# Kernel tuning notes

Hardware: AMD Instinct MI355X
Metric: run time of the kernel (lower is better)

The kernel has to match this reference:

```python
import jax, jax.numpy as jnp
import numpy as np

B, T, N, F_, KH, D, KD = 16, 12, 325, 64, 4, 16, 3  # batch, time, nodes, feat, heads, head_dim, diffusion steps
H = KH // 2
EPS = 1e-5


def setup_inputs() -> dict:
    key = jax.random.key(0)
    ks = jax.random.split(key, 16)
    lin = lambda k: (jax.random.normal(k, (F_, F_), jnp.float32) * 0.02)
    return {
        "x": jax.random.normal(ks[0], (B, T, N, F_), jnp.float32),
        "A": jax.random.uniform(ks[1], (KD, N, N), jnp.float32),
        "AT": jax.random.uniform(ks[2], (KD, N, N), jnp.float32),
        "Wq": lin(ks[3]), "bq": jnp.zeros((F_,), jnp.float32),
        "Wk": lin(ks[4]), "bk": jnp.zeros((F_,), jnp.float32),
        "Wks": lin(ks[5]), "bks": jnp.zeros((F_,), jnp.float32),
        "Wv": lin(ks[6]), "bv": jnp.zeros((F_,), jnp.float32),
        "Wvs": lin(ks[7]), "bvs": jnp.zeros((F_,), jnp.float32),
        "Wdi": jax.random.normal(ks[8], (H, KD, N, N), jnp.float32) * 0.05,
        "Wdo": jax.random.normal(ks[9], (H, KD, N, N), jnp.float32) * 0.05,
        "Wf1": lin(ks[10]), "bf1": jnp.zeros((F_,), jnp.float32),
        "Wf2": lin(ks[11]), "bf2": jnp.zeros((F_,), jnp.float32),
        "g_ln": jnp.ones((F_,), jnp.float32), "b_ln": jnp.zeros((F_,), jnp.float32),
    }


def _heads(y):
    # [B,T,N,F] -> [KH,B,T,N,D]  (torch.split along -1 then stack on dim 0)
    return y.reshape(B, T, N, KH, D).transpose(3, 0, 1, 2, 4)


def _attn_half(q, k, ks_, v, vs, bias):
    # q,k,ks_,v,vs: [H,B,T,N,D]; bias: [H,1,1,N,N]
    scale = 1.0 / jnp.sqrt(jnp.float32(D))
    e = jnp.einsum('hbtnd,hbtmd->hbtnm', q, k) * scale + bias
    es = jax.nn.sigmoid((q * ks_).sum(-1, keepdims=True) * scale)  # [H,B,T,N,1]
    e = e - e.max(-1, keepdims=True)
    ex = jnp.exp(e)
    a = ex / (es + ex.sum(-1, keepdims=True))  # sigmoid-augmented softmax
    out = jnp.einsum('hbtnm,hbtmd->hbtnd', a, v)
    return out + vs - a.sum(-1, keepdims=True) * vs


def reference(x, A, AT, Wq, bq, Wk, bk, Wks, bks, Wv, bv, Wvs, bvs,
              Wdi, Wdo, Wf1, bf1, Wf2, bf2, g_ln, b_ln):
    q = _heads(x @ Wq.T + bq)
    k = _heads(x @ Wk.T + bk)
    ks_ = _heads(x @ Wks.T + bks)
    v = _heads(x @ Wv.T + bv)
    vs = _heads(x @ Wvs.T + bvs)

    # DCN graph-diffusion bias: sum_j W[h,j] * A[j] -> [H,1,1,N,N]
    bias_i = jnp.einsum('hknm,knm->hnm', Wdi, A)[:, None, None]
    bias_o = jnp.einsum('hknm,knm->hnm', Wdo, AT)[:, None, None]

    vi = _attn_half(q[:H], k[:H], ks_[:H], v[:H], vs[:H], bias_i)
    vo = _attn_half(q[H:], k[H:], ks_[H:], v[H:], vs[H:], bias_o)

    val = jnp.concatenate([vi, vo], 0)  # [KH,B,T,N,D]
    val = val.transpose(1, 2, 3, 0, 4).reshape(B, T, N, F_)

    h = jax.nn.gelu(val @ Wf1.T + bf1, approximate=False) @ Wf2.T + bf2
    h = h + x

    mu = h.mean(-1, keepdims=True)
    var = ((h - mu) ** 2).mean(-1, keepdims=True)
    return g_ln * (h - mu) / jnp.sqrt(var + EPS) + b_ln
```

## Files before the change

kernel.cpp:

```cpp
#include <hip/hip_runtime.h>
#include <hip/hip_bf16.h>
#include <math.h>

#define NN 325
#define FD 64
#define KH 4
#define DH 16
#define BT 192
#define NN2 (NN*NN)
#define PST (NN*DH)
#define SSTR 340
#define BSTR 352
#define VTS  352
#define VSLICE (16*VTS)
#define HSTR 72
#define NPROJ 975
#define NBIAS ((KH*NN*BSTR + 255)/256)
#define NPAD  (KH*BT)
#define LOG2E 1.44269504088896f

typedef __attribute__((ext_vector_type(8))) short short8;
typedef __attribute__((ext_vector_type(4))) float f32x4;

union U8 { uint4 u; short8 s; ushort us[8]; };
__device__ inline short8 lds8(const ushort* p){ U8 t; t.u = *(const uint4*)p; return t.s; }
__device__ inline float b2f(ushort v){ return __uint_as_float(((unsigned)v) << 16); }
__device__ inline ushort f2b(float f){
  unsigned u = __float_as_uint(f);
  u += 0x7fff + ((u >> 16) & 1);
  return (ushort)(u >> 16);
}
__device__ inline unsigned pk2(float a, float b){
  union { __hip_bfloat162 h; unsigned u; } t;
  t.h = __float22bfloat162_rn(float2{a, b});
  return t.u;
}
__device__ inline short8 cvt8(const float* p){
  float4 u = ((const float4*)p)[0], v = ((const float4*)p)[1];
  U8 t;
  t.us[0]=f2b(u.x); t.us[1]=f2b(u.y); t.us[2]=f2b(u.z); t.us[3]=f2b(u.w);
  t.us[4]=f2b(v.x); t.us[5]=f2b(v.y); t.us[6]=f2b(v.z); t.us[7]=f2b(v.w);
  return t.s;
}

__global__ __launch_bounds__(256) void wpack_kernel(
    const float* __restrict__ Wq,  const float* __restrict__ bq,
    const float* __restrict__ Wk,  const float* __restrict__ bk,
    const float* __restrict__ Wks, const float* __restrict__ bks,
    const float* __restrict__ Wv,  const float* __restrict__ bv,
    const float* __restrict__ Wvs, const float* __restrict__ bvs,
    const float* __restrict__ Wf1, const float* __restrict__ Wf2,
    ushort* __restrict__ Wcat, float* __restrict__ bcat){
  int blk = blockIdx.x;
  const float* Ws[7] = {Wq, Wk, Wks, Wv, Wvs, Wf1, Wf2};
  const float* bs[5] = {bq, bk, bks, bv, bvs};
  int f = blk * 64 + (threadIdx.x >> 2);
  int c0 = (threadIdx.x & 3) * 8;
  const float* wr = Ws[blk] + (f & 63) * 64;
  unsigned* dst = (unsigned*)Wcat + f * 32 + c0;
  #pragma unroll
  for (int c = 0; c < 8; ++c)
    dst[c] = f2b(wr[2*(c0+c)]) | ((unsigned)f2b(wr[2*(c0+c)+1]) << 16);
  if (blk < 5 && (threadIdx.x & 3) == 0) bcat[f] = bs[blk][f & 63];
}

__global__ __launch_bounds__(256) void prep_kernel(
    const float* __restrict__ x, const ushort* __restrict__ Wcat,
    const float* __restrict__ bcat, ushort* __restrict__ proj,
    ushort* __restrict__ vt,
    const float* __restrict__ Wdi, const float* __restrict__ Wdo,
    const float* __restrict__ A,   const float* __restrict__ AT,
    float* __restrict__ biasP){
  int bid = blockIdx.x, tid = threadIdx.x;
  if (bid < NPROJ){
    int lane = tid & 63, wid = tid >> 6;
    int r0 = bid * 64 + wid * 16;
    int m = lane & 15, g = lane >> 4;
    int gr = r0 + m;
    int bt = gr / NN, n = gr - bt * NN;
    const float* xr = x + (size_t)gr * 64 + g * 8;
    short8 xb0 = cvt8(xr);
    short8 xb1 = cvt8(xr + 32);
    for (int ct = 0; ct < 20; ++ct){
      short8 w0 = lds8(Wcat + ((size_t)(ct*16 + m) * 64 + g * 8));
      short8 w1 = lds8(Wcat + ((size_t)(ct*16 + m) * 64 + g * 8 + 32));
      float4 b4 = *(const float4*)(bcat + ct*16 + 4*g);
      f32x4 acc = {b4.x, b4.y, b4.z, b4.w};
      acc = __builtin_amdgcn_mfma_f32_16x16x32_bf16(w0, xb0, acc, 0, 0, 0);
      acc = __builtin_amdgcn_mfma_f32_16x16x32_bf16(w1, xb1, acc, 0, 0, 0);
      if (ct >= 12 && ct < 16){
        ushort* vs = vt + (size_t)((ct-12)*BT + bt) * VSLICE + n;
        #pragma unroll
        for (int rg = 0; rg < 4; ++rg)
          vs[(size_t)(4*g + rg) * VTS] = f2b(acc[rg]);
      } else {
        float sc = (ct < 4) ? 0.25f * LOG2E : 1.0f;
        uint2 w;
        w.x = pk2(acc[0]*sc, acc[1]*sc);
        w.y = pk2(acc[2]*sc, acc[3]*sc);
        *(uint2*)(proj + ((size_t)ct * BT + bt) * PST + n*16 + 4*g) = w;
      }
    }
  } else if (bid < NPROJ + NBIAS){
    int idx = (bid - NPROJ) * 256 + tid;
    if (idx >= KH * NN * BSTR) return;
    int h = idx / (NN * BSTR), rem = idx - h * (NN * BSTR);
    int n = rem / BSTR, m = rem - n * BSTR;
    float s = -1e30f;
    if (m < NN){
      int r = n * NN + m;
      s = 0.f;
      if (h < 2){
        #pragma unroll
        for (int k = 0; k < 3; ++k) s += Wdi[(h*3 + k)*NN2 + r] * A[k*NN2 + r];
      } else {
        int h2 = h - 2;
        #pragma unroll
        for (int k = 0; k < 3; ++k) s += Wdo[(h2*3 + k)*NN2 + r] * AT[k*NN2 + r];
      }
      s *= LOG2E;
    }
    biasP[idx] = s;
  } else {
    int slice = bid - NPROJ - NBIAS;
    ushort* vs = vt + (size_t)slice * VSLICE;
    if (tid < 432){
      int d = tid / 27, c = NN + tid % 27;
      vs[(size_t)d * VTS + c] = 0;
    }
  }
}

__global__ __launch_bounds__(256, 4) void attn_kernel(
    const ushort* __restrict__ proj, const float* __restrict__ biasP,
    const ushort* __restrict__ vt, ushort* __restrict__ val){
  __shared__ float S[16 * SSTR];
  __shared__ float part[4][16][16];
  __shared__ float rstat[16][2];
  int bhid = blockIdx.x, qt = blockIdx.y;
  int h = bhid / BT, bt = bhid - h * BT;
  int tid = threadIdx.x, lane = tid & 63, wid = tid >> 6;
  const ushort* qb  = proj + (size_t)((0*KH + h)*BT + bt) * PST;
  const ushort* kb  = proj + (size_t)((1*KH + h)*BT + bt) * PST;
  const ushort* ksb = proj + (size_t)((2*KH + h)*BT + bt) * PST;
  const ushort* vsb = proj + (size_t)((4*KH + h)*BT + bt) * PST;
  const ushort* vtg = vt + (size_t)(h*BT + bt) * VSLICE;

  int m = lane & 15, g = lane >> 4;
  short8 zero = {0,0,0,0,0,0,0,0};

  short8 aq = (g < 2) ? lds8(qb + ((size_t)(qt*16 + m) * 16 + g * 8)) : zero;
  short8 kf[6];
  #pragma unroll
  for (int i = 0; i < 6; ++i){
    int ct = wid + 4*i;
    kf[i] = (ct < 21 && g < 2) ? lds8(kb + ((size_t)(ct*16 + m) * 16 + g * 8)) : zero;
  }
  short8 vf[3];
  #pragma unroll
  for (int i = 0; i < 3; ++i){
    int tt = wid + 4*i;
    vf[i] = (tt < 11) ? lds8(vtg + (size_t)m * VTS + tt*32 + g*8) : zero;
  }
  int r = tid >> 4, c = tid & 15;
  int n = qt * 16 + r;
  int nb = min(n, NN - 1);
  const float* bp = biasP + (size_t)(h*NN + nb) * BSTR;
  float4 b4[6];
  #pragma unroll
  for (int j = 0; j < 6; ++j){
    int m0 = c * 4 + 64 * j;
    b4[j] = (m0 < 336) ? *(const float4*)(bp + m0) : make_float4(0.f,0.f,0.f,0.f);
  }
  float qv  = b2f(qb[(size_t)nb * 16 + c]);
  float kv  = b2f(ksb[(size_t)nb * 16 + c]);
  float vsv = b2f(vsb[(size_t)nb * 16 + c]);

  #pragma unroll
  for (int i = 0; i < 6; ++i){
    int ct = wid + 4*i;
    if (ct < 21){
      f32x4 acc = {0.f, 0.f, 0.f, 0.f};
      acc = __builtin_amdgcn_mfma_f32_16x16x32_bf16(aq, kf[i], acc, 0, 0, 0);
      #pragma unroll
      for (int rg = 0; rg < 4; ++rg)
        S[(g*4 + rg)*SSTR + ct*16 + m] = acc[rg];
    }
  }
  __syncthreads();

  {
    float* sr = S + r * SSTR;
    ushort* pr = (ushort*)sr;
    float sum = 0.f;
    #pragma unroll
    for (int j = 0; j < 6; ++j){
      int m0 = c * 4 + 64 * j;
      if (m0 < 336){
        float4 s4 = *(const float4*)(sr + m0);
        float e0 = __builtin_amdgcn_exp2f(s4.x + b4[j].x);
        float e1 = __builtin_amdgcn_exp2f(s4.y + b4[j].y);
        float e2 = __builtin_amdgcn_exp2f(s4.z + b4[j].z);
        float e3 = __builtin_amdgcn_exp2f(s4.w + b4[j].w);
        sum += (e0 + e1) + (e2 + e3);
        uint2 w;
        w.x = pk2(e0, e1);
        w.y = pk2(e2, e3);
        *(uint2*)(pr + m0) = w;
      }
    }
    float dp = qv * kv;
    dp += __shfl_xor(dp, 1, 64); dp += __shfl_xor(dp, 2, 64);
    dp += __shfl_xor(dp, 4, 64); dp += __shfl_xor(dp, 8, 64);
    sum += __shfl_xor(sum, 1, 64); sum += __shfl_xor(sum, 2, 64);
    sum += __shfl_xor(sum, 4, 64); sum += __shfl_xor(sum, 8, 64);
    if (c == 0){
      float esv = __builtin_amdgcn_rcpf(1.f + __builtin_amdgcn_exp2f(-dp));
      float iv  = __builtin_amdgcn_rcpf(esv + sum);
      rstat[r][0] = iv; rstat[r][1] = 1.f - sum * iv;
    }
  }
  __syncthreads();

  {
    const ushort* prow = (const ushort*)S + (size_t)m * (SSTR * 2);
    f32x4 acc = {0.f, 0.f, 0.f, 0.f};
    #pragma unroll
    for (int i = 0; i < 3; ++i){
      int tt = wid + 4*i;
      if (tt < 11){
        short8 ap = (tt == 10 && g >= 2) ? zero : lds8(prow + tt*32 + g*8);
        acc = __builtin_amdgcn_mfma_f32_16x16x32_bf16(ap, vf[i], acc, 0, 0, 0);
      }
    }
    #pragma unroll
    for (int rg = 0; rg < 4; ++rg)
      part[wid][g*4 + rg][m] = acc[rg];
  }
  __syncthreads();

  if (n < NN){
    float s = part[0][r][c] + part[1][r][c] + part[2][r][c] + part[3][r][c];
    float res = s * rstat[r][0] + rstat[r][1] * vsv;
    val[((size_t)bt * NN + n) * FD + h * 16 + c] = f2b(res);
  }
}

__global__ __launch_bounds__(256) void ffn_kernel(
    const ushort* __restrict__ val, const float* __restrict__ x,
    const ushort* __restrict__ Wf1b, const float* __restrict__ bf1,
    const ushort* __restrict__ Wf2b, const float* __restrict__ bf2,
    const float* __restrict__ g_ln, const float* __restrict__ b_ln,
    float* __restrict__ out){
  __shared__ ushort hs[4][16 * HSTR];
  int tid = threadIdx.x, lane = tid & 63, wid = tid >> 6;
  int m = lane & 15, g = lane >> 4;
  int r0 = blockIdx.x * 64 + wid * 16;
  int row = r0 + m;

  short8 vb0 = lds8(val + ((size_t)row * 64 + g * 8));
  short8 vb1 = lds8(val + ((size_t)row * 64 + g * 8 + 32));

  #pragma unroll
  for (int ct = 0; ct < 4; ++ct){
    short8 w0 = lds8(Wf1b + ((size_t)(ct*16 + m) * 64 + g * 8));
    short8 w1 = lds8(Wf1b + ((size_t)(ct*16 + m) * 64 + g * 8 + 32));
    float4 b4 = *(const float4*)(bf1 + ct*16 + 4*g);
    f32x4 acc = {b4.x, b4.y, b4.z, b4.w};
    acc = __builtin_amdgcn_mfma_f32_16x16x32_bf16(w0, vb0, acc, 0, 0, 0);
    acc = __builtin_amdgcn_mfma_f32_16x16x32_bf16(w1, vb1, acc, 0, 0, 0);
    uint2 w;
    float g0 = 0.5f*acc[0]*(1.f + erff(acc[0]*0.70710678118654752f));
    float g1 = 0.5f*acc[1]*(1.f + erff(acc[1]*0.70710678118654752f));
    float g2 = 0.5f*acc[2]*(1.f + erff(acc[2]*0.70710678118654752f));
    float g3 = 0.5f*acc[3]*(1.f + erff(acc[3]*0.70710678118654752f));
    w.x = pk2(g0, g1); w.y = pk2(g2, g3);
    *(uint2*)&hs[wid][m * HSTR + ct*16 + 4*g] = w;
  }
  asm volatile("s_waitcnt lgkmcnt(0)" ::: "memory");
  short8 h0 = lds8(&hs[wid][m * HSTR + g * 8]);
  short8 h1 = lds8(&hs[wid][m * HSTR + g * 8 + 32]);

  float t[4][4];
  #pragma unroll
  for (int ct = 0; ct < 4; ++ct){
    short8 w0 = lds8(Wf2b + ((size_t)(ct*16 + m) * 64 + g * 8));
    short8 w1 = lds8(Wf2b + ((size_t)(ct*16 + m) * 64 + g * 8 + 32));
    float4 b4 = *(const float4*)(bf2 + ct*16 + 4*g);
    f32x4 acc = {b4.x, b4.y, b4.z, b4.w};
    acc = __builtin_amdgcn_mfma_f32_16x16x32_bf16(w0, h0, acc, 0, 0, 0);
    acc = __builtin_amdgcn_mfma_f32_16x16x32_bf16(w1, h1, acc, 0, 0, 0);
    float4 xr = *(const float4*)(x + (size_t)row * 64 + ct*16 + 4*g);
    t[ct][0] = acc[0] + xr.x; t[ct][1] = acc[1] + xr.y;
    t[ct][2] = acc[2] + xr.z; t[ct][3] = acc[3] + xr.w;
  }
  float s = 0.f;
  #pragma unroll
  for (int ct = 0; ct < 4; ++ct) s += (t[ct][0]+t[ct][1]) + (t[ct][2]+t[ct][3]);
  s += __shfl_xor(s, 16, 64); s += __shfl_xor(s, 32, 64);
  float mu = s * (1.f/64.f);
  float v = 0.f;
  #pragma unroll
  for (int ct = 0; ct < 4; ++ct){
    #pragma unroll
    for (int rg = 0; rg < 4; ++rg){ float d = t[ct][rg] - mu; v += d*d; }
  }
  v += __shfl_xor(v, 16, 64); v += __shfl_xor(v, 32, 64);
  float rs = rsqrtf(v * (1.f/64.f) + 1e-5f);
  #pragma unroll
  for (int ct = 0; ct < 4; ++ct){
    float4 g4 = *(const float4*)(g_ln + ct*16 + 4*g);
    float4 bb = *(const float4*)(b_ln + ct*16 + 4*g);
    float4 o;
    o.x = g4.x*(t[ct][0]-mu)*rs + bb.x;
    o.y = g4.y*(t[ct][1]-mu)*rs + bb.y;
    o.z = g4.z*(t[ct][2]-mu)*rs + bb.z;
    o.w = g4.w*(t[ct][3]-mu)*rs + bb.w;
    *(float4*)(out + (size_t)row * 64 + ct*16 + 4*g) = o;
  }
}

extern "C" void kernel_launch(void* const* d_in, const int* in_sizes, int n_in,
                              void* d_out, int out_size, void* d_ws, size_t ws_size,
                              hipStream_t stream) {
  const float* x    = (const float*)d_in[0];
  const float* A    = (const float*)d_in[1];
  const float* AT   = (const float*)d_in[2];
  const float* Wq   = (const float*)d_in[3];
  const float* bq   = (const float*)d_in[4];
  const float* Wk   = (const float*)d_in[5];
  const float* bk   = (const float*)d_in[6];
  const float* Wks  = (const float*)d_in[7];
  const float* bks  = (const float*)d_in[8];
  const float* Wv   = (const float*)d_in[9];
  const float* bv   = (const float*)d_in[10];
  const float* Wvs  = (const float*)d_in[11];
  const float* bvs  = (const float*)d_in[12];
  const float* Wdi  = (const float*)d_in[13];
  const float* Wdo  = (const float*)d_in[14];
  const float* Wf1  = (const float*)d_in[15];
  const float* bf1  = (const float*)d_in[16];
  const float* Wf2  = (const float*)d_in[17];
  const float* bf2  = (const float*)d_in[18];
  const float* g_ln = (const float*)d_in[19];
  const float* b_ln = (const float*)d_in[20];
  float* out = (float*)d_out;

  float* ws = (float*)d_ws;
  ushort* proj  = (ushort*)ws;
  float*  biasP = ws + 9984000;
  ushort* val   = (ushort*)(ws + 10441600);
  ushort* vt    = (ushort*)(ws + 12438400);
  ushort* Wcat  = (ushort*)(ws + 14601088);
  float*  bcat  = ws + 14615424;
  ushort* Wf1b  = Wcat + 320*64;
  ushort* Wf2b  = Wcat + 384*64;

  wpack_kernel<<<7, 256, 0, stream>>>(Wq, bq, Wk, bk, Wks, bks,
                                      Wv, bv, Wvs, bvs, Wf1, Wf2, Wcat, bcat);
  prep_kernel<<<NPROJ + NBIAS + NPAD, 256, 0, stream>>>(
      x, Wcat, bcat, proj, vt, Wdi, Wdo, A, AT, biasP);
  attn_kernel<<<dim3(KH*BT, 21), 256, 0, stream>>>(proj, biasP, vt, val);
  ffn_kernel<<<975, 256, 0, stream>>>(val, x, Wf1b, bf1, Wf2b, bf2,
                                      g_ln, b_ln, out);
}
```

Baseline: 197.0 us.

## Fold bias into QK MFMA via identity operand, one wave per query tile

The attention kernel now gives each wave its own 16-row query tile and computes scores with a single MFMA per column tile. The K dimension's upper half multiplies a precomputed bf16 identity matrix by the bf16 graph bias, so the bias add is folded into the matrix multiply. Scores are exponentiated directly from registers into per-wave LDS, and the block-wide barriers and cross-wave partial reductions are removed. The bias is now stored as bf16 instead of fp32, which halves its traffic but lowers the precision of the bias term.

```diff
diff --git a/kernel.cpp b/kernel.cpp
--- a/kernel.cpp
+++ b/kernel.cpp
@@ -9,13 +9,12 @@
 #define BT 192
 #define NN2 (NN*NN)
 #define PST (NN*DH)
-#define SSTR 340
-#define BSTR 352
 #define VTS  352
 #define VSLICE (16*VTS)
 #define HSTR 72
+#define PLW 352
 #define NPROJ 975
-#define NBIAS ((KH*NN*BSTR + 255)/256)
+#define NBIAS 1848
 #define NPAD  (KH*BT)
 #define LOG2E 1.44269504088896f
 
@@ -50,8 +49,19 @@
     const float* __restrict__ Wv,  const float* __restrict__ bv,
     const float* __restrict__ Wvs, const float* __restrict__ bvs,
     const float* __restrict__ Wf1, const float* __restrict__ Wf2,
-    ushort* __restrict__ Wcat, float* __restrict__ bcat){
+    ushort* __restrict__ Wcat, float* __restrict__ bcat,
+    ushort* __restrict__ idT){
   int blk = blockIdx.x;
+  if (blk == 7){
+    for (int e = threadIdx.x; e < 672; e += 256){
+      int l = e & 31, mm = l & 15, gg = l >> 4;
+      U8 t;
+      #pragma unroll
+      for (int j = 0; j < 8; ++j) t.us[j] = (mm == gg*8 + j) ? (ushort)0x3F80 : (ushort)0;
+      *(uint4*)(idT + (size_t)e*8) = t.u;
+    }
+    return;
+  }
   const float* Ws[7] = {Wq, Wk, Wks, Wv, Wvs, Wf1, Wf2};
   const float* bs[5] = {bq, bk, bks, bv, bvs};
   int f = blk * 64 + (threadIdx.x >> 2);
@@ -70,7 +80,7 @@
     ushort* __restrict__ vt,
     const float* __restrict__ Wdi, const float* __restrict__ Wdo,
     const float* __restrict__ A,   const float* __restrict__ AT,
-    float* __restrict__ biasP){
+    ushort* __restrict__ biasB){
   int bid = blockIdx.x, tid = threadIdx.x;
   if (bid < NPROJ){
     int lane = tid & 63, wid = tid >> 6;
@@ -103,12 +113,12 @@
     }
   } else if (bid < NPROJ + NBIAS){
     int idx = (bid - NPROJ) * 256 + tid;
-    if (idx >= KH * NN * BSTR) return;
-    int h = idx / (NN * BSTR), rem = idx - h * (NN * BSTR);
-    int n = rem / BSTR, m = rem - n * BSTR;
+    int h = idx / 118272;
+    int rem = idx - h * 118272;
+    int n = rem / 352, mc = rem - n * 352;
     float s = -1e30f;
-    if (m < NN){
-      int r = n * NN + m;
+    if (n < NN && mc < NN){
+      int r = n * NN + mc;
       s = 0.f;
       if (h < 2){
         #pragma unroll
@@ -120,7 +130,7 @@
       }
       s *= LOG2E;
     }
-    biasP[idx] = s;
+    biasB[idx] = f2b(s);
   } else {
     int slice = bid - NPROJ - NBIAS;
     ushort* vs = vt + (size_t)slice * VSLICE;
@@ -131,118 +141,88 @@
   }
 }
 
-__global__ __launch_bounds__(256, 4) void attn_kernel(
-    const ushort* __restrict__ proj, const float* __restrict__ biasP,
-    const ushort* __restrict__ vt, ushort* __restrict__ val){
-  __shared__ float S[16 * SSTR];
-  __shared__ float part[4][16][16];
-  __shared__ float rstat[16][2];
-  int bhid = blockIdx.x, qt = blockIdx.y;
-  int h = bhid / BT, bt = bhid - h * BT;
+__global__ __launch_bounds__(256, 3) void attn_kernel(
+    const ushort* __restrict__ proj, const ushort* __restrict__ biasB,
+    const ushort* __restrict__ idT, const ushort* __restrict__ vt,
+    ushort* __restrict__ val){
+  __shared__ __align__(16) ushort Pl[4][16*PLW];
   int tid = threadIdx.x, lane = tid & 63, wid = tid >> 6;
+  int tile = blockIdx.x * 4 + wid;
+  int qt = tile % 21, bh = tile / 21;
+  int h = bh / BT, bt = bh - h * BT;
+  int m = lane & 15, g = lane >> 4;
+
   const ushort* qb  = proj + (size_t)((0*KH + h)*BT + bt) * PST;
   const ushort* kb  = proj + (size_t)((1*KH + h)*BT + bt) * PST;
   const ushort* ksb = proj + (size_t)((2*KH + h)*BT + bt) * PST;
   const ushort* vsb = proj + (size_t)((4*KH + h)*BT + bt) * PST;
-  const ushort* vtg = vt + (size_t)(h*BT + bt) * VSLICE;
-
-  int m = lane & 15, g = lane >> 4;
-  short8 zero = {0,0,0,0,0,0,0,0};
-
-  short8 aq = (g < 2) ? lds8(qb + ((size_t)(qt*16 + m) * 16 + g * 8)) : zero;
-  short8 kf[6];
-  #pragma unroll
-  for (int i = 0; i < 6; ++i){
-    int ct = wid + 4*i;
-    kf[i] = (ct < 21 && g < 2) ? lds8(kb + ((size_t)(ct*16 + m) * 16 + g * 8)) : zero;
-  }
-  short8 vf[3];
-  #pragma unroll
-  for (int i = 0; i < 3; ++i){
-    int tt = wid + 4*i;
-    vf[i] = (tt < 11) ? lds8(vtg + (size_t)m * VTS + tt*32 + g*8) : zero;
-  }
-  int r = tid >> 4, c = tid & 15;
-  int n = qt * 16 + r;
-  int nb = min(n, NN - 1);
-  const float* bp = biasP + (size_t)(h*NN + nb) * BSTR;
-  float4 b4[6];
-  #pragma unroll
-  for (int j = 0; j < 6; ++j){
-    int m0 = c * 4 + 64 * j;
-    b4[j] = (m0 < 336) ? *(const float4*)(bp + m0) : make_float4(0.f,0.f,0.f,0.f);
-  }
-  float qv  = b2f(qb[(size_t)nb * 16 + c]);
-  float kv  = b2f(ksb[(size_t)nb * 16 + c]);
-  float vsv = b2f(vsb[(size_t)nb * 16 + c]);
-
-  #pragma unroll
-  for (int i = 0; i < 6; ++i){
-    int ct = wid + 4*i;
-    if (ct < 21){
-      f32x4 acc = {0.f, 0.f, 0.f, 0.f};
-      acc = __builtin_amdgcn_mfma_f32_16x16x32_bf16(aq, kf[i], acc, 0, 0, 0);
-      #pragma unroll
-      for (int rg = 0; rg < 4; ++rg)
-        S[(g*4 + rg)*SSTR + ct*16 + m] = acc[rg];
-    }
-  }
-  __syncthreads();
-
-  {
-    float* sr = S + r * SSTR;
-    ushort* pr = (ushort*)sr;
-    float sum = 0.f;
-    #pragma unroll
-    for (int j = 0; j < 6; ++j){
-      int m0 = c * 4 + 64 * j;
-      if (m0 < 336){
-        float4 s4 = *(const float4*)(sr + m0);
-        float e0 = __builtin_amdgcn_exp2f(s4.x + b4[j].x);
-        float e1 = __builtin_amdgcn_exp2f(s4.y + b4[j].y);
-        float e2 = __builtin_amdgcn_exp2f(s4.z + b4[j].z);
-        float e3 = __builtin_amdgcn_exp2f(s4.w + b4[j].w);
-        sum += (e0 + e1) + (e2 + e3);
-        uint2 w;
-        w.x = pk2(e0, e1);
-        w.y = pk2(e2, e3);
-        *(uint2*)(pr + m0) = w;
-      }
-    }
-    float dp = qv * kv;
-    dp += __shfl_xor(dp, 1, 64); dp += __shfl_xor(dp, 2, 64);
-    dp += __shfl_xor(dp, 4, 64); dp += __shfl_xor(dp, 8, 64);
-    sum += __shfl_xor(sum, 1, 64); sum += __shfl_xor(sum, 2, 64);
-    sum += __shfl_xor(sum, 4, 64); sum += __shfl_xor(sum, 8, 64);
-    if (c == 0){
-      float esv = __builtin_amdgcn_rcpf(1.f + __builtin_amdgcn_exp2f(-dp));
-      float iv  = __builtin_amdgcn_rcpf(esv + sum);
-      rstat[r][0] = iv; rstat[r][1] = 1.f - sum * iv;
-    }
-  }
-  __syncthreads();
-
-  {
-    const ushort* prow = (const ushort*)S + (size_t)m * (SSTR * 2);
+
+  const ushort* pa0 = (g < 2) ? (kb + m*16 + g*8) : (idT + (size_t)(lane & 31)*8);
+  const ushort* pb0 = (g < 2)
+      ? (qb + (size_t)(qt*16 + m)*16 + g*8)
+      : (biasB + (size_t)(h*336 + qt*16 + m)*352 + (g-2)*8);
+  int bstep = (g < 2) ? 0 : 16;
+
+  ushort* Pw = &Pl[wid][m*PLW + g*4];
+  float rowsum = 0.f;
+  #pragma unroll
+  for (int ct = 0; ct < 21; ++ct){
+    short8 a = lds8(pa0 + ct*256);
+    short8 b = lds8(pb0 + ct*bstep);
     f32x4 acc = {0.f, 0.f, 0.f, 0.f};
-    #pragma unroll
-    for (int i = 0; i < 3; ++i){
-      int tt = wid + 4*i;
-      if (tt < 11){
-        short8 ap = (tt == 10 && g >= 2) ? zero : lds8(prow + tt*32 + g*8);
-        acc = __builtin_amdgcn_mfma_f32_16x16x32_bf16(ap, vf[i], acc, 0, 0, 0);
-      }
-    }
-    #pragma unroll
-    for (int rg = 0; rg < 4; ++rg)
-      part[wid][g*4 + rg][m] = acc[rg];
-  }
-  __syncthreads();
-
-  if (n < NN){
-    float s = part[0][r][c] + part[1][r][c] + part[2][r][c] + part[3][r][c];
-    float res = s * rstat[r][0] + rstat[r][1] * vsv;
-    val[((size_t)bt * NN + n) * FD + h * 16 + c] = f2b(res);
+    acc = __builtin_amdgcn_mfma_f32_16x16x32_bf16(a, b, acc, 0, 0, 0);
+    float e0 = __builtin_amdgcn_exp2f(acc[0]);
+    float e1 = __builtin_amdgcn_exp2f(acc[1]);
+    float e2 = __builtin_amdgcn_exp2f(acc[2]);
+    float e3 = __builtin_amdgcn_exp2f(acc[3]);
+    rowsum += (e0 + e1) + (e2 + e3);
+    uint2 w; w.x = pk2(e0, e1); w.y = pk2(e2, e3);
+    *(uint2*)(Pw + ct*16) = w;
+  }
+  { uint2 z; z.x = 0u; z.y = 0u; *(uint2*)(Pw + 336) = z; }
+
+  rowsum += __shfl_xor(rowsum, 16, 64);
+  rowsum += __shfl_xor(rowsum, 32, 64);
+
+  int nq = qt*16 + m, nb = min(nq, NN-1);
+  uint2 qw = *(const uint2*)(qb + (size_t)nb*16 + g*4);
+  uint2 kw = *(const uint2*)(ksb + (size_t)nb*16 + g*4);
+  float dp = b2f((ushort)(qw.x & 0xffff)) * b2f((ushort)(kw.x & 0xffff))
+           + b2f((ushort)(qw.x >> 16))    * b2f((ushort)(kw.x >> 16))
+           + b2f((ushort)(qw.y & 0xffff)) * b2f((ushort)(kw.y & 0xffff))
+           + b2f((ushort)(qw.y >> 16))    * b2f((ushort)(kw.y >> 16));
+  dp += __shfl_xor(dp, 16, 64);
+  dp += __shfl_xor(dp, 32, 64);
+  float esv  = __builtin_amdgcn_rcpf(1.f + __builtin_amdgcn_exp2f(-dp));
+  float inv  = __builtin_amdgcn_rcpf(esv + rowsum);
+  float beta = 1.f - rowsum * inv;
+
+  asm volatile("s_waitcnt lgkmcnt(0)" ::: "memory");
+
+  const ushort* Pr  = &Pl[wid][m*PLW + g*8];
+  const ushort* vtg = vt + (size_t)(h*BT + bt)*VSLICE + (size_t)m*VTS + g*8;
+  f32x4 o = {0.f, 0.f, 0.f, 0.f};
+  #pragma unroll
+  for (int tt = 0; tt < 11; ++tt){
+    short8 pf = lds8(Pr + tt*32);
+    short8 vf = lds8(vtg + tt*32);
+    o = __builtin_amdgcn_mfma_f32_16x16x32_bf16(pf, vf, o, 0, 0, 0);
+  }
+
+  int sb = g << 4;
+  float invr[4], betr[4];
+  #pragma unroll
+  for (int rg = 0; rg < 4; ++rg){
+    invr[rg] = __uint_as_float(__builtin_amdgcn_ds_bpermute(sb + rg*4, __float_as_uint(inv)));
+    betr[rg] = __uint_as_float(__builtin_amdgcn_ds_bpermute(sb + rg*4, __float_as_uint(beta)));
+  }
+  #pragma unroll
+  for (int rg = 0; rg < 4; ++rg){
+    int n = qt*16 + 4*g + rg;
+    int nc = min(n, NN-1);
+    float vsx = b2f(vsb[(size_t)nc*16 + m]);
+    float res = o[rg]*invr[rg] + betr[rg]*vsx;
+    if (n < NN) val[((size_t)bt*NN + n)*FD + h*16 + m] = f2b(res);
   }
 }
 
@@ -348,7 +328,8 @@
 
   float* ws = (float*)d_ws;
   ushort* proj  = (ushort*)ws;
-  float*  biasP = ws + 9984000;
+  ushort* biasB = (ushort*)(ws + 9984000);
+  ushort* idT   = biasB + 473088;
   ushort* val   = (ushort*)(ws + 10441600);
   ushort* vt    = (ushort*)(ws + 12438400);
   ushort* Wcat  = (ushort*)(ws + 14601088);
@@ -356,11 +337,11 @@
   ushort* Wf1b  = Wcat + 320*64;
   ushort* Wf2b  = Wcat + 384*64;
 
-  wpack_kernel<<<7, 256, 0, stream>>>(Wq, bq, Wk, bk, Wks, bks,
-                                      Wv, bv, Wvs, bvs, Wf1, Wf2, Wcat, bcat);
+  wpack_kernel<<<8, 256, 0, stream>>>(Wq, bq, Wk, bk, Wks, bks,
+                                      Wv, bv, Wvs, bvs, Wf1, Wf2, Wcat, bcat, idT);
   prep_kernel<<<NPROJ + NBIAS + NPAD, 256, 0, stream>>>(
-      x, Wcat, bcat, proj, vt, Wdi, Wdo, A, AT, biasP);
-  attn_kernel<<<dim3(KH*BT, 21), 256, 0, stream>>>(proj, biasP, vt, val);
+      x, Wcat, bcat, proj, vt, Wdi, Wdo, A, AT, biasB);
+  attn_kernel<<<4032, 256, 0, stream>>>(proj, biasB, idT, vt, val);
   ffn_kernel<<<975, 256, 0, stream>>>(val, x, Wf1b, bf1, Wf2b, bf2,
                                       g_ln, b_ln, out);
 }
```

New measurement: 193.3 us. No clear change (-1.9%).
